# Kernel optimization log

Hardware: AMD Instinct MI355X
Metric: run time of the kernel (lower is better)

The kernel has to match this reference:

```python
import jax, jax.numpy as jnp
import numpy as np

EPS = 1e-4  # ReEig clamp


def _spectral(X, f):
    # eigendecompose symmetric X and apply f to eigenvalues: V diag(f(w)) V^T
    w, v = jnp.linalg.eigh(X)
    return jnp.einsum('...ij,...j,...kj->...ik', v, f(w), v)


def _bimap(W, X):
    # W @ X @ W.T with W [out,in], X [b,in,in]
    return jnp.einsum('ij,bjk,lk->bil', W, X, W)


def setup_inputs() -> dict:
    key = jax.random.key(0)
    k1, k2, k3, k4 = jax.random.split(key, 4)
    B = 262144
    vech = jax.random.normal(k1, (B, 6), dtype=jnp.float32)
    # Stiefel init: Q factor of a Gaussian (orthonormal columns)
    W1 = jnp.linalg.qr(jax.random.normal(k2, (5, 3), dtype=jnp.float32))[0]
    W2 = jnp.linalg.qr(jax.random.normal(k3, (7, 5), dtype=jnp.float32))[0]
    W3 = jnp.linalg.qr(jax.random.normal(k4, (9, 7), dtype=jnp.float32))[0]
    return {"vech": vech, "W1": W1, "W2": W2, "W3": W3}


def reference(vech, W1, W2, W3):
    k = 3
    B = vech.shape[0]
    iu = jnp.triu_indices(k)
    X = jnp.zeros((B, k, k), dtype=vech.dtype).at[:, iu[0], iu[1]].set(vech)
    d = jnp.diagonal(X, axis1=-2, axis2=-1)  # [B,3]
    X = X + jnp.swapaxes(X, -2, -1) - d[..., :, None] * jnp.eye(k, dtype=vech.dtype)
    # SPDNet chain
    X = _spectral(X, jnp.exp)                      # ExpEig -> [B,3,3]
    X = _bimap(W1, X)                              # [B,5,5]
    X = _spectral(X, lambda w: jnp.maximum(w, EPS))  # ReEig
    X = _bimap(W2, X)                              # [B,7,7]
    X = _spectral(X, lambda w: jnp.maximum(w, EPS))
    X = _bimap(W3, X)                              # [B,9,9]
    X = _spectral(X, lambda w: jnp.maximum(w, EPS))
    return X
```

## Files before the change

kernel.cpp:

```cpp
#include <hip/hip_runtime.h>

#define EPSV 1e-4f

typedef float v4f __attribute__((ext_vector_type(4)));

__device__ __forceinline__ void jrot(float& app, float& aqq, float& apq,
                                     float& arp, float& arq,
                                     float& vap, float& vaq,
                                     float& vbp, float& vbq,
                                     float& vcp, float& vcq) {
  const float apq0 = apq;
  float tau = (aqq - app) / (2.0f * apq0);
  float t = copysignf(1.0f / (fabsf(tau) + sqrtf(fmaf(tau, tau, 1.0f))), tau);
  if (apq0 == 0.0f) t = 0.0f;
  const float c = rsqrtf(fmaf(t, t, 1.0f));
  const float s = t * c;
  const float d = t * apq0;
  app -= d; aqq += d; apq = 0.0f;
  const float rp = arp, rq = arq;
  arp = c * rp - s * rq;
  arq = s * rp + c * rq;
  float x, y;
  x = vap; y = vaq; vap = c * x - s * y; vaq = s * x + c * y;
  x = vbp; y = vbq; vbp = c * x - s * y; vbq = s * x + c * y;
  x = vcp; y = vcq; vcp = c * x - s * y; vcq = s * x + c * y;
}

__global__ __launch_bounds__(256, 4) void spd_decoder_kernel(
    const float* __restrict__ vech, const float* __restrict__ W1,
    const float* __restrict__ W2, const float* __restrict__ W3,
    float* __restrict__ out, int B) {
  __shared__ float Tsh[21];
  __shared__ float Msh[27];
  __shared__ __align__(16) float buf[4][1296];

  const int tid = threadIdx.x;

  if (tid < 21) {
    const int r = tid / 3, c = tid % 3;
    float acc = 0.f;
#pragma unroll
    for (int j = 0; j < 5; ++j) acc += W2[r * 5 + j] * W1[j * 3 + c];
    Tsh[tid] = acc;
  }
  __syncthreads();
  if (tid < 27) {
    const int r = tid / 3, c = tid % 3;
    float acc = 0.f;
#pragma unroll
    for (int j = 0; j < 7; ++j) acc += W3[r * 7 + j] * Tsh[j * 3 + c];
    Msh[tid] = acc;
  }
  __syncthreads();

  const int e = blockIdx.x * 256 + tid;
  const float2* vp = reinterpret_cast<const float2*>(vech + (size_t)e * 6);
  const float2 p0 = vp[0], p1 = vp[1], p2 = vp[2];
  float a00 = p0.x, a01 = p0.y, a02 = p1.x, a11 = p1.y, a12 = p2.x, a22 = p2.y;

  float v00 = 1.f, v01 = 0.f, v02 = 0.f;
  float v10 = 0.f, v11 = 1.f, v12 = 0.f;
  float v20 = 0.f, v21 = 0.f, v22 = 1.f;
#pragma unroll
  for (int sweep = 0; sweep < 5; ++sweep) {
    jrot(a00, a11, a01, a02, a12, v00, v01, v10, v11, v20, v21);
    jrot(a00, a22, a02, a01, a12, v00, v02, v10, v12, v20, v22);
    jrot(a11, a22, a12, a01, a02, v01, v02, v11, v12, v21, v22);
  }

  const float e0 = expf(a00) - EPSV;
  const float e1 = expf(a11) - EPSV;
  const float e2 = expf(a22) - EPSV;

  float g0[9], g1[9], g2[9];
#pragma unroll
  for (int i = 0; i < 9; ++i) {
    const float m0 = Msh[i * 3 + 0], m1 = Msh[i * 3 + 1], m2 = Msh[i * 3 + 2];
    g0[i] = fmaf(m0, v00, fmaf(m1, v10, m2 * v20));
    g1[i] = fmaf(m0, v01, fmaf(m1, v11, m2 * v21));
    g2[i] = fmaf(m0, v02, fmaf(m1, v12, m2 * v22));
  }

  const int w = tid >> 6, l = tid & 63;
  float* wbuf = &buf[w][0];
  const size_t base = (size_t)(blockIdx.x * 256 + w * 64) * 81;

#pragma unroll
  for (int h = 0; h < 4; ++h) {
    if ((l >> 4) == h) {
      const int ll = l & 15;
      float* dst = wbuf + ll * 81;
#pragma unroll
      for (int i = 0; i < 9; ++i) {
        const float t0 = e0 * g0[i], t1 = e1 * g1[i], t2 = e2 * g2[i];
#pragma unroll
        for (int j = 0; j < 9; ++j) {
          float val = fmaf(t0, g0[j], fmaf(t1, g1[j], t2 * g2[j]));
          if (i == j) val += EPSV;
          dst[i * 9 + j] = val;
        }
      }
    }
    asm volatile("s_waitcnt lgkmcnt(0)" ::: "memory");

    const size_t sb = base + (size_t)h * 1296;
    const v4f* rbuf = reinterpret_cast<const v4f*>(wbuf);
    v4f* outv = reinterpret_cast<v4f*>(out + sb);
#pragma unroll
    for (int it = 0; it < 5; ++it)
      __builtin_nontemporal_store(rbuf[it * 64 + l], outv + it * 64 + l);
    if (l < 4) __builtin_nontemporal_store(rbuf[320 + l], outv + 320 + l);
  }
}

extern "C" void kernel_launch(void* const* d_in, const int* in_sizes, int n_in,
                              void* d_out, int out_size, void* d_ws, size_t ws_size,
                              hipStream_t stream) {
  const float* vech = (const float*)d_in[0];
  const float* W1 = (const float*)d_in[1];
  const float* W2 = (const float*)d_in[2];
  const float* W3 = (const float*)d_in[3];
  float* out = (float*)d_out;
  const int B = in_sizes[0] / 6;
  dim3 grid(B / 256), block(256);
  hipLaunchKernelGGL(spd_decoder_kernel, grid, block, 0, stream,
                     vech, W1, W2, W3, out, B);
}
```

Before: 24.46 us.

## Use single-wave blocks with two matrices per thread and full-wave LDS staging

Restructures the kernel so each 64-thread block handles 128 matrices, two per thread. All lanes write their 9x9 results to LDS at once instead of in four 16-lane phases, then the wave streams them out. Block barriers become LDS waitcnts, and the vech loads are hoisted ahead of the weight-product setup. It also uses fast rcp/rsq intrinsics, exp2 for the exponent, and cuts Jacobi sweeps from five to four. Fewer sweeps and approximate reciprocals may reduce eigen-decomposition accuracy, and the per-block 20 KB LDS buffer may limit occupancy.

```diff
diff --git a/kernel.cpp b/kernel.cpp
--- a/kernel.cpp
+++ b/kernel.cpp
@@ -1,6 +1,7 @@
 #include <hip/hip_runtime.h>
 
 #define EPSV 1e-4f
+#define LOG2E 1.4426950408889634f
 
 typedef float v4f __attribute__((ext_vector_type(4)));
 
@@ -10,106 +11,109 @@
                                      float& vbp, float& vbq,
                                      float& vcp, float& vcq) {
   const float apq0 = apq;
-  float tau = (aqq - app) / (2.0f * apq0);
-  float t = copysignf(1.0f / (fabsf(tau) + sqrtf(fmaf(tau, tau, 1.0f))), tau);
+  const float tau = (aqq - app) * (0.5f * __builtin_amdgcn_rcpf(apq0));
+  float t = copysignf(
+      __builtin_amdgcn_rcpf(fabsf(tau) + sqrtf(fmaf(tau, tau, 1.0f))), tau);
   if (apq0 == 0.0f) t = 0.0f;
-  const float c = rsqrtf(fmaf(t, t, 1.0f));
+  const float c = __builtin_amdgcn_rsqf(fmaf(t, t, 1.0f));
   const float s = t * c;
   const float d = t * apq0;
   app -= d; aqq += d; apq = 0.0f;
-  const float rp = arp, rq = arq;
-  arp = c * rp - s * rq;
-  arq = s * rp + c * rq;
   float x, y;
-  x = vap; y = vaq; vap = c * x - s * y; vaq = s * x + c * y;
-  x = vbp; y = vbq; vbp = c * x - s * y; vbq = s * x + c * y;
-  x = vcp; y = vcq; vcp = c * x - s * y; vcq = s * x + c * y;
+  x = arp; y = arq; arp = fmaf(c, x, -(s * y)); arq = fmaf(s, x, c * y);
+  x = vap; y = vaq; vap = fmaf(c, x, -(s * y)); vaq = fmaf(s, x, c * y);
+  x = vbp; y = vbq; vbp = fmaf(c, x, -(s * y)); vbq = fmaf(s, x, c * y);
+  x = vcp; y = vcq; vcp = fmaf(c, x, -(s * y)); vcq = fmaf(s, x, c * y);
 }
 
-__global__ __launch_bounds__(256, 4) void spd_decoder_kernel(
+__global__ __launch_bounds__(64, 2) void spd_decoder_kernel(
     const float* __restrict__ vech, const float* __restrict__ W1,
     const float* __restrict__ W2, const float* __restrict__ W3,
     float* __restrict__ out, int B) {
   __shared__ float Tsh[21];
   __shared__ float Msh[27];
-  __shared__ __align__(16) float buf[4][1296];
+  __shared__ __align__(16) float buf[64 * 81];
 
-  const int tid = threadIdx.x;
+  const int l = threadIdx.x;
 
-  if (tid < 21) {
-    const int r = tid / 3, c = tid % 3;
+  const int ebase = blockIdx.x * 128 + l;
+  const float2* va = reinterpret_cast<const float2*>(vech + (size_t)ebase * 6);
+  const float2* vb =
+      reinterpret_cast<const float2*>(vech + (size_t)(ebase + 64) * 6);
+  const float2 A0 = va[0], A1 = va[1], A2 = va[2];
+  const float2 B0 = vb[0], B1 = vb[1], B2 = vb[2];
+
+  if (l < 21) {
+    const int r = l / 3, c = l % 3;
     float acc = 0.f;
 #pragma unroll
     for (int j = 0; j < 5; ++j) acc += W2[r * 5 + j] * W1[j * 3 + c];
-    Tsh[tid] = acc;
+    Tsh[l] = acc;
   }
-  __syncthreads();
-  if (tid < 27) {
-    const int r = tid / 3, c = tid % 3;
+  asm volatile("s_waitcnt lgkmcnt(0)" ::: "memory");
+  if (l < 27) {
+    const int r = l / 3, c = l % 3;
     float acc = 0.f;
 #pragma unroll
     for (int j = 0; j < 7; ++j) acc += W3[r * 7 + j] * Tsh[j * 3 + c];
-    Msh[tid] = acc;
+    Msh[l] = acc;
   }
-  __syncthreads();
+  asm volatile("s_waitcnt lgkmcnt(0)" ::: "memory");
 
-  const int e = blockIdx.x * 256 + tid;
-  const float2* vp = reinterpret_cast<const float2*>(vech + (size_t)e * 6);
-  const float2 p0 = vp[0], p1 = vp[1], p2 = vp[2];
-  float a00 = p0.x, a01 = p0.y, a02 = p1.x, a11 = p1.y, a12 = p2.x, a22 = p2.y;
+  float M[27];
+#pragma unroll
+  for (int i = 0; i < 27; ++i) M[i] = Msh[i];
 
-  float v00 = 1.f, v01 = 0.f, v02 = 0.f;
-  float v10 = 0.f, v11 = 1.f, v12 = 0.f;
-  float v20 = 0.f, v21 = 0.f, v22 = 1.f;
-#pragma unroll
-  for (int sweep = 0; sweep < 5; ++sweep) {
-    jrot(a00, a11, a01, a02, a12, v00, v01, v10, v11, v20, v21);
-    jrot(a00, a22, a02, a01, a12, v00, v02, v10, v12, v20, v22);
-    jrot(a11, a22, a12, a01, a02, v01, v02, v11, v12, v21, v22);
-  }
-
-  const float e0 = expf(a00) - EPSV;
-  const float e1 = expf(a11) - EPSV;
-  const float e2 = expf(a22) - EPSV;
-
-  float g0[9], g1[9], g2[9];
-#pragma unroll
-  for (int i = 0; i < 9; ++i) {
-    const float m0 = Msh[i * 3 + 0], m1 = Msh[i * 3 + 1], m2 = Msh[i * 3 + 2];
-    g0[i] = fmaf(m0, v00, fmaf(m1, v10, m2 * v20));
-    g1[i] = fmaf(m0, v01, fmaf(m1, v11, m2 * v21));
-    g2[i] = fmaf(m0, v02, fmaf(m1, v12, m2 * v22));
-  }
-
-  const int w = tid >> 6, l = tid & 63;
-  float* wbuf = &buf[w][0];
-  const size_t base = (size_t)(blockIdx.x * 256 + w * 64) * 81;
+  float* const dst = buf + l * 81;
+  const v4f* const rb = reinterpret_cast<const v4f*>(buf);
 
 #pragma unroll
-  for (int h = 0; h < 4; ++h) {
-    if ((l >> 4) == h) {
-      const int ll = l & 15;
-      float* dst = wbuf + ll * 81;
+  for (int p = 0; p < 2; ++p) {
+    const float2 q0 = p ? B0 : A0, q1 = p ? B1 : A1, q2 = p ? B2 : A2;
+    float a00 = q0.x, a01 = q0.y, a02 = q1.x, a11 = q1.y, a12 = q2.x,
+          a22 = q2.y;
+
+    float v00 = 1.f, v01 = 0.f, v02 = 0.f;
+    float v10 = 0.f, v11 = 1.f, v12 = 0.f;
+    float v20 = 0.f, v21 = 0.f, v22 = 1.f;
 #pragma unroll
-      for (int i = 0; i < 9; ++i) {
-        const float t0 = e0 * g0[i], t1 = e1 * g1[i], t2 = e2 * g2[i];
+    for (int sweep = 0; sweep < 4; ++sweep) {
+      jrot(a00, a11, a01, a02, a12, v00, v01, v10, v11, v20, v21);
+      jrot(a00, a22, a02, a01, a12, v00, v02, v10, v12, v20, v22);
+      jrot(a11, a22, a12, a01, a02, v01, v02, v11, v12, v21, v22);
+    }
+
+    const float e0 = exp2f(a00 * LOG2E) - EPSV;
+    const float e1 = exp2f(a11 * LOG2E) - EPSV;
+    const float e2 = exp2f(a22 * LOG2E) - EPSV;
+
+    float g0[9], g1[9], g2[9];
 #pragma unroll
-        for (int j = 0; j < 9; ++j) {
-          float val = fmaf(t0, g0[j], fmaf(t1, g1[j], t2 * g2[j]));
-          if (i == j) val += EPSV;
-          dst[i * 9 + j] = val;
-        }
+    for (int i = 0; i < 9; ++i) {
+      const float m0 = M[i * 3 + 0], m1 = M[i * 3 + 1], m2 = M[i * 3 + 2];
+      g0[i] = fmaf(m0, v00, fmaf(m1, v10, m2 * v20));
+      g1[i] = fmaf(m0, v01, fmaf(m1, v11, m2 * v21));
+      g2[i] = fmaf(m0, v02, fmaf(m1, v12, m2 * v22));
+    }
+
+#pragma unroll
+    for (int i = 0; i < 9; ++i) {
+      const float t0 = e0 * g0[i], t1 = e1 * g1[i], t2 = e2 * g2[i];
+#pragma unroll
+      for (int j = 0; j < 9; ++j) {
+        float val = fmaf(t0, g0[j], fmaf(t1, g1[j], t2 * g2[j]));
+        if (i == j) val += EPSV;
+        dst[i * 9 + j] = val;
       }
     }
     asm volatile("s_waitcnt lgkmcnt(0)" ::: "memory");
 
-    const size_t sb = base + (size_t)h * 1296;
-    const v4f* rbuf = reinterpret_cast<const v4f*>(wbuf);
-    v4f* outv = reinterpret_cast<v4f*>(out + sb);
+    const size_t fb = (size_t)(blockIdx.x * 128 + p * 64) * 81;
+    v4f* op = reinterpret_cast<v4f*>(out + fb);
 #pragma unroll
-    for (int it = 0; it < 5; ++it)
-      __builtin_nontemporal_store(rbuf[it * 64 + l], outv + it * 64 + l);
-    if (l < 4) __builtin_nontemporal_store(rbuf[320 + l], outv + 320 + l);
+    for (int it = 0; it < 20; ++it)
+      __builtin_nontemporal_store(rb[it * 64 + l], op + it * 64 + l);
+    if (l < 16) __builtin_nontemporal_store(rb[1280 + l], op + 1280 + l);
   }
 }
 
@@ -122,7 +126,7 @@
   const float* W3 = (const float*)d_in[3];
   float* out = (float*)d_out;
   const int B = in_sizes[0] / 6;
-  dim3 grid(B / 256), block(256);
+  dim3 grid(B / 128), block(64);
   hipLaunchKernelGGL(spd_decoder_kernel, grid, block, 0, stream,
                      vech, W1, W2, W3, out, B);
 }
```

Result: slower. 25.58 us (+4.6%).
